# Kernel optimization log

Measured on AMD Instinct MI355X. Metric: run time of the kernel, lower is better.

The kernel has to match this reference:

```python
import jax, jax.numpy as jnp
import numpy as np

N, E = 40000, 640000          # nodes, edges (avg degree 16)
IN_N, IN_E = 8 + 768, 2       # in_dim_node + in_dim_text, in_dim_edge
H, OUT, NC, L = 128, 128, 5, 2
EPS_BN, EPS_DEN = 1e-5, 1e-6


def setup_inputs() -> dict:
    key = jax.random.key(0)
    ks = jax.random.split(key, 16)
    w = lambda k, shape: jax.random.normal(k, shape, jnp.float32) * 0.05
    return {
        "node_feat": jax.random.normal(ks[0], (N, IN_N), jnp.float32),
        "edge_feat": jax.random.normal(ks[1], (E, IN_E), jnp.float32),
        "src": jax.random.randint(ks[2], (E,), 0, N),
        "dst": jax.random.randint(ks[3], (E,), 0, N),
        "enc_nw": w(ks[4], (IN_N, H)), "enc_nb": jnp.zeros((H,), jnp.float32),
        "enc_ew": w(ks[5], (IN_E, H)), "enc_eb": jnp.zeros((H,), jnp.float32),
        # per layer: 5 linears (order A, B, C, D, E)
        "lin_w": w(ks[6], (L, 5, H, H)), "lin_b": jnp.zeros((L, 5, H), jnp.float32),
        "bnh_g": jnp.ones((L, H), jnp.float32), "bnh_b": jnp.zeros((L, H), jnp.float32),
        "bne_g": jnp.ones((L, H), jnp.float32), "bne_b": jnp.zeros((L, H), jnp.float32),
        "mlp_w1": w(ks[7], (H, OUT)), "mlp_b1": jnp.zeros((OUT,), jnp.float32),
        "mlp_w2": w(ks[8], (OUT, NC)), "mlp_b2": jnp.zeros((NC,), jnp.float32),
    }


def _bn(x, g, b):
    # training-mode BatchNorm1d: batch stats, biased variance, eps=1e-5
    m = jnp.mean(x, axis=0)
    v = jnp.var(x, axis=0)
    return (x - m) * jax.lax.rsqrt(v + EPS_BN) * g + b


def reference(node_feat, edge_feat, src, dst, enc_nw, enc_nb, enc_ew, enc_eb,
              lin_w, lin_b, bnh_g, bnh_b, bne_g, bne_b,
              mlp_w1, mlp_b1, mlp_w2, mlp_b2):
    n = node_feat.shape[0]
    h = node_feat @ enc_nw + enc_nb          # [N, H]
    e = edge_feat @ enc_ew + enc_eb          # [E, H]
    for l in range(L):
        Ah = h @ lin_w[l, 0] + lin_b[l, 0]
        Bh = h @ lin_w[l, 1] + lin_b[l, 1]
        Ce = e @ lin_w[l, 2] + lin_b[l, 2]
        Dh = h @ lin_w[l, 3] + lin_b[l, 3]
        Eh = h @ lin_w[l, 4] + lin_b[l, 4]
        e_new = Ce + Dh[src] + Eh[dst]       # [E, H] edge gate logits
        sigma = jax.nn.sigmoid(e_new)
        num = jax.ops.segment_sum(sigma * Bh[src], dst, num_segments=n)
        den = jax.ops.segment_sum(sigma, dst, num_segments=n)
        h_new = Ah + num / (den + EPS_DEN)
        h = jax.nn.relu(_bn(h_new, bnh_g[l], bnh_b[l]))
        e = jax.nn.relu(_bn(e_new, bne_g[l], bne_b[l]))
    # MLP readout per node (dropout p=0 -> identity)
    logits = jax.nn.relu(h @ mlp_w1 + mlp_b1) @ mlp_w2 + mlp_b2
    return logits
```

## Files before the change

### kernel.cpp

```cpp
#include <hip/hip_runtime.h>
#include <math.h>

#define NN 40000
#define NE 640000
#define KIN 776
#define HH 128
#define NCLS 5

typedef __attribute__((ext_vector_type(8))) short bf16x8;
typedef __attribute__((ext_vector_type(4))) short bf16x4;
typedef __attribute__((ext_vector_type(4))) float f32x4;

__device__ __forceinline__ float bf2f(short u) {
    return __uint_as_float(((unsigned)(unsigned short)u) << 16);
}
__device__ __forceinline__ short f2bf(float f) {
    unsigned u = __float_as_uint(f);
    u += 0x7fffu + ((u >> 16) & 1u);
    return (short)(u >> 16);
}

template<int NSTEP, bool TAIL8>
__global__ __launch_bounds__(256)
void mfma_gemm(const float* __restrict__ Af, const short* __restrict__ Wp,
               const float* __restrict__ bias, short* __restrict__ Cb, int K)
{
    const int lane = threadIdx.x & 63;
    const int wave = threadIdx.x >> 6;
    const int q = lane >> 4;
    const int c16 = lane & 15;
    const int row = blockIdx.x * 64 + wave * 16 + c16;

    f32x4 acc[8];
#pragma unroll
    for (int n = 0; n < 8; ++n) acc[n] = (f32x4){0.f, 0.f, 0.f, 0.f};

    for (int kt = 0; kt < NSTEP; ++kt) {
        bf16x8 afrag;
        const int kbase = kt * 32 + q * 8;
        if (!TAIL8 || kt < NSTEP - 1 || q == 0) {
            const float* p = Af + (size_t)row * K + kbase;
            const float4 x = *(const float4*)p;
            const float4 y = *(const float4*)(p + 4);
            afrag[0] = f2bf(x.x); afrag[1] = f2bf(x.y);
            afrag[2] = f2bf(x.z); afrag[3] = f2bf(x.w);
            afrag[4] = f2bf(y.x); afrag[5] = f2bf(y.y);
            afrag[6] = f2bf(y.z); afrag[7] = f2bf(y.w);
        } else {
#pragma unroll
            for (int j = 0; j < 8; ++j) afrag[j] = 0;
        }
        const int kb = kt * 4 + q;
#pragma unroll
        for (int n = 0; n < 8; ++n) {
            const bf16x8 wfrag =
                *(const bf16x8*)(Wp + (size_t)kb * 1024 + (n * 16 + c16) * 8);
            acc[n] = __builtin_amdgcn_mfma_f32_16x16x32_bf16(wfrag, afrag, acc[n], 0, 0, 0);
        }
    }
#pragma unroll
    for (int n = 0; n < 8; ++n) {
        const int col = n * 16 + q * 4;
        const float4 b4 = *(const float4*)(bias + col);
        bf16x4 o;
        o[0] = f2bf(acc[n][0] + b4.x); o[1] = f2bf(acc[n][1] + b4.y);
        o[2] = f2bf(acc[n][2] + b4.z); o[3] = f2bf(acc[n][3] + b4.w);
        *(bf16x4*)(Cb + (size_t)row * HH + col) = o;
    }
}

template<bool ABN>
__global__ __launch_bounds__(256, 2)
void fused4_k(const short* __restrict__ hb, const float* __restrict__ hf,
              const float* __restrict__ bnp,
              const short* __restrict__ w0, const short* __restrict__ w1,
              const short* __restrict__ w2, const short* __restrict__ w3,
              const float* __restrict__ b0, const float* __restrict__ b1,
              const float* __restrict__ b2, const float* __restrict__ b3,
              float* __restrict__ Ah, short* __restrict__ Bh,
              short* __restrict__ Dh, short* __restrict__ Eh)
{
    const int lane = threadIdx.x & 63;
    const int wave = threadIdx.x >> 6;
    const int q = lane >> 4;
    const int c16 = lane & 15;
    const int row = blockIdx.x * 64 + wave * 16 + c16;

    f32x4 acc[4][8];
#pragma unroll
    for (int t = 0; t < 4; ++t)
#pragma unroll
        for (int n = 0; n < 8; ++n) acc[t][n] = (f32x4){0.f, 0.f, 0.f, 0.f};

    const short* const ws[4] = {w0, w1, w2, w3};
#pragma unroll
    for (int kt = 0; kt < 4; ++kt) {
        const int kbase = kt * 32 + q * 8;
        bf16x8 afrag;
        if (!ABN) {
            afrag = *(const bf16x8*)(hb + (size_t)row * HH + kbase);
        } else {
            const float* p = hf + (size_t)row * HH + kbase;
            const float4 x = *(const float4*)p;
            const float4 y = *(const float4*)(p + 4);
            const float4 s0 = *(const float4*)(bnp + kbase);
            const float4 s1 = *(const float4*)(bnp + kbase + 4);
            const float4 t0 = *(const float4*)(bnp + HH + kbase);
            const float4 t1 = *(const float4*)(bnp + HH + kbase + 4);
            const float xv[8] = {x.x, x.y, x.z, x.w, y.x, y.y, y.z, y.w};
            const float scv[8] = {s0.x, s0.y, s0.z, s0.w, s1.x, s1.y, s1.z, s1.w};
            const float shv[8] = {t0.x, t0.y, t0.z, t0.w, t1.x, t1.y, t1.z, t1.w};
#pragma unroll
            for (int j = 0; j < 8; ++j)
                afrag[j] = f2bf(fmaxf(fmaf(xv[j], scv[j], shv[j]), 0.f));
        }
        const int kb = kt * 4 + q;
#pragma unroll
        for (int t = 0; t < 4; ++t)
#pragma unroll
            for (int n = 0; n < 8; ++n) {
                const bf16x8 wfrag =
                    *(const bf16x8*)(ws[t] + (size_t)kb * 1024 + (n * 16 + c16) * 8);
                acc[t][n] = __builtin_amdgcn_mfma_f32_16x16x32_bf16(wfrag, afrag, acc[t][n], 0, 0, 0);
            }
    }

    const float* const bs[4] = {b0, b1, b2, b3};
#pragma unroll
    for (int t = 0; t < 4; ++t) {
#pragma unroll
        for (int n = 0; n < 8; ++n) {
            const int col = n * 16 + q * 4;
            const float4 b4 = *(const float4*)(bs[t] + col);
            const float v[4] = {acc[t][n][0] + b4.x, acc[t][n][1] + b4.y,
                                acc[t][n][2] + b4.z, acc[t][n][3] + b4.w};
            if (t == 0) {
                *(float4*)(Ah + (size_t)row * HH + col) = make_float4(v[0], v[1], v[2], v[3]);
            } else {
                bf16x4 o;
#pragma unroll
                for (int j = 0; j < 4; ++j) o[j] = f2bf(v[j]);
                short* dstp = (t == 1) ? Bh : ((t == 2) ? Dh : Eh);
                *(bf16x4*)(dstp + (size_t)row * HH + col) = o;
            }
        }
    }
}

__global__ __launch_bounds__(256)
void edge1seg_k(const float* __restrict__ ef, const int* __restrict__ eidx,
                const int* __restrict__ src_s, const int* __restrict__ rowptr,
                const float* __restrict__ G,
                const short* __restrict__ Dh, const short* __restrict__ Eh,
                const short* __restrict__ Bh, const float* __restrict__ Ah,
                float* __restrict__ hnew, float* __restrict__ pbuf)
{
    const int wv = threadIdx.x >> 6;
    const int lane = threadIdx.x & 63;
    const int slot = lane >> 4;
    const int cg = lane & 15;
    const int col = cg * 8;
    const int n0 = (blockIdx.x * 4 + wv) * 8;

    const float4 g00 = *(const float4*)(G + col);
    const float4 g01 = *(const float4*)(G + col + 4);
    const float4 g10 = *(const float4*)(G + HH + col);
    const float4 g11 = *(const float4*)(G + HH + col + 4);
    const float4 gb0 = *(const float4*)(G + 2 * HH + col);
    const float4 gb1 = *(const float4*)(G + 2 * HH + col + 4);
    const float G0v[8] = {g00.x, g00.y, g00.z, g00.w, g01.x, g01.y, g01.z, g01.w};
    const float G1v[8] = {g10.x, g10.y, g10.z, g10.w, g11.x, g11.y, g11.z, g11.w};
    const float GBv[8] = {gb0.x, gb0.y, gb0.z, gb0.w, gb1.x, gb1.y, gb1.z, gb1.w};

    float esa[8] = {}, esq[8] = {};

    for (int nn = 0; nn < 8; ++nn) {
        const int n = n0 + nn;
        const int k0 = rowptr[n], k1 = rowptr[n + 1];
        const bf16x8 ehn = *(const bf16x8*)(Eh + (size_t)n * HH + col);
        float ehv[8];
#pragma unroll
        for (int j = 0; j < 8; ++j) ehv[j] = bf2f(ehn[j]);
        float num[8] = {}, den[8] = {};
        for (int k = k0 + slot; k < k1; k += 4) {
            const int e = eidx[k];
            const int s = src_s[k];
            const float f0 = ef[(size_t)e * 2];
            const float f1 = ef[(size_t)e * 2 + 1];
            const bf16x8 dh = *(const bf16x8*)(Dh + (size_t)s * HH + col);
            const bf16x8 bh = *(const bf16x8*)(Bh + (size_t)s * HH + col);
#pragma unroll
            for (int j = 0; j < 8; ++j) {
                const float v = fmaf(f0, G0v[j], fmaf(f1, G1v[j], GBv[j]))
                                + bf2f(dh[j]) + ehv[j];
                esa[j] += v; esq[j] += v * v;
                const float sg = 1.f / (1.f + __expf(-v));
                den[j] += sg;
                num[j] = fmaf(sg, bf2f(bh[j]), num[j]);
            }
        }
#pragma unroll
        for (int j = 0; j < 8; ++j) {
            num[j] += __shfl_xor(num[j], 16, 64);
            den[j] += __shfl_xor(den[j], 16, 64);
            num[j] += __shfl_xor(num[j], 32, 64);
            den[j] += __shfl_xor(den[j], 32, 64);
        }
        if (slot == 0) {
            const size_t idx = (size_t)n * HH + col;
            const float4 a0 = *(const float4*)(Ah + idx);
            const float4 a1 = *(const float4*)(Ah + idx + 4);
            const float av[8] = {a0.x, a0.y, a0.z, a0.w, a1.x, a1.y, a1.z, a1.w};
            float x[8];
#pragma unroll
            for (int j = 0; j < 8; ++j) x[j] = av[j] + num[j] / (den[j] + 1e-6f);
            *(float4*)(hnew + idx) = make_float4(x[0], x[1], x[2], x[3]);
            *(float4*)(hnew + idx + 4) = make_float4(x[4], x[5], x[6], x[7]);
        }
    }

    __shared__ float sred[16][136];
    const int er = threadIdx.x >> 4;
    const int slotp = (blockIdx.x & 63) * 256;
#pragma unroll
    for (int j = 0; j < 8; ++j) sred[er][col + j] = esa[j];
    __syncthreads();
    for (int s2 = 8; s2 > 0; s2 >>= 1) {
        if (er < s2)
#pragma unroll
            for (int j = 0; j < 8; ++j) sred[er][col + j] += sred[er + s2][col + j];
        __syncthreads();
    }
    if (er == 0)
#pragma unroll
        for (int j = 0; j < 8; ++j) atomicAdd(pbuf + slotp + col + j, sred[0][col + j]);
    __syncthreads();
#pragma unroll
    for (int j = 0; j < 8; ++j) sred[er][col + j] = esq[j];
    __syncthreads();
    for (int s2 = 8; s2 > 0; s2 >>= 1) {
        if (er < s2)
#pragma unroll
            for (int j = 0; j < 8; ++j) sred[er][col + j] += sred[er + s2][col + j];
        __syncthreads();
    }
    if (er == 0)
#pragma unroll
        for (int j = 0; j < 8; ++j) atomicAdd(pbuf + slotp + 128 + col + j, sred[0][col + j]);
}

__global__ void gm_k(const float* __restrict__ G, const float* __restrict__ bnpe,
                     float* __restrict__ Gm)
{
    const int c = threadIdx.x;
    const float sc = bnpe[c], sh = bnpe[128 + c];
    Gm[c] = G[c] * sc;
    Gm[128 + c] = G[HH + c] * sc;
    Gm[256 + c] = fmaf(G[2 * HH + c], sc, sh);
    Gm[384 + c] = sc;
}

__global__ __launch_bounds__(256)
void edge2_k(const int* __restrict__ eidx, const float* __restrict__ ef,
             const float* __restrict__ Gm,
             const short* __restrict__ Dh0, const short* __restrict__ Eh0,
             const short* __restrict__ Dh1, const short* __restrict__ Eh1,
             const int* __restrict__ src_s, const int* __restrict__ dst_s,
             const short* __restrict__ Wp, const float* __restrict__ bias,
             short* __restrict__ enew)
{
    const int lane = threadIdx.x & 63;
    const int wave = threadIdx.x >> 6;
    const int q = lane >> 4;
    const int c16 = lane & 15;
    const int row0 = blockIdx.x * 128 + wave * 16 + c16;
    const int row1 = row0 + 64;

    const int s0 = src_s[row0], d0 = dst_s[row0];
    const int s1 = src_s[row1], d1 = dst_s[row1];
    const int e0 = eidx[row0], e1 = eidx[row1];
    const float2 ef0 = *(const float2*)(ef + (size_t)e0 * 2);
    const float2 ef1 = *(const float2*)(ef + (size_t)e1 * 2);

    f32x4 acc[2][8];
#pragma unroll
    for (int n = 0; n < 8; ++n) {
        const int col = n * 16 + q * 4;
        const float4 b4 = *(const float4*)(bias + col);
        const bf16x4 dh0 = *(const bf16x4*)(Dh1 + (size_t)s0 * HH + col);
        const bf16x4 eh0 = *(const bf16x4*)(Eh1 + (size_t)d0 * HH + col);
        const bf16x4 dh1 = *(const bf16x4*)(Dh1 + (size_t)s1 * HH + col);
        const bf16x4 eh1 = *(const bf16x4*)(Eh1 + (size_t)d1 * HH + col);
        const float bb[4] = {b4.x, b4.y, b4.z, b4.w};
#pragma unroll
        for (int j = 0; j < 4; ++j) {
            acc[0][n][j] = bb[j] + bf2f(dh0[j]) + bf2f(eh0[j]);
            acc[1][n][j] = bb[j] + bf2f(dh1[j]) + bf2f(eh1[j]);
        }
    }

#pragma unroll
    for (int kt = 0; kt < 4; ++kt) {
        const int kbase = kt * 32 + q * 8;
        const float4 p0 = *(const float4*)(Gm + kbase);
        const float4 p1 = *(const float4*)(Gm + kbase + 4);
        const float4 p2 = *(const float4*)(Gm + 128 + kbase);
        const float4 p3 = *(const float4*)(Gm + 128 + kbase + 4);
        const float4 p4 = *(const float4*)(Gm + 256 + kbase);
        const float4 p5 = *(const float4*)(Gm + 256 + kbase + 4);
        const float4 p6 = *(const float4*)(Gm + 384 + kbase);
        const float4 p7 = *(const float4*)(Gm + 384 + kbase + 4);
        const float g0s[8] = {p0.x, p0.y, p0.z, p0.w, p1.x, p1.y, p1.z, p1.w};
        const float g1s[8] = {p2.x, p2.y, p2.z, p2.w, p3.x, p3.y, p3.z, p3.w};
        const float gbs[8] = {p4.x, p4.y, p4.z, p4.w, p5.x, p5.y, p5.z, p5.w};
        const float scv[8] = {p6.x, p6.y, p6.z, p6.w, p7.x, p7.y, p7.z, p7.w};
        const bf16x8 dA0 = *(const bf16x8*)(Dh0 + (size_t)s0 * HH + kbase);
        const bf16x8 eA0 = *(const bf16x8*)(Eh0 + (size_t)d0 * HH + kbase);
        const bf16x8 dA1 = *(const bf16x8*)(Dh0 + (size_t)s1 * HH + kbase);
        const bf16x8 eA1 = *(const bf16x8*)(Eh0 + (size_t)d1 * HH + kbase);
        bf16x8 a0, a1;
#pragma unroll
        for (int j = 0; j < 8; ++j) {
            float t0 = fmaf(scv[j], bf2f(dA0[j]) + bf2f(eA0[j]), gbs[j]);
            t0 = fmaf(ef0.x, g0s[j], fmaf(ef0.y, g1s[j], t0));
            a0[j] = f2bf(fmaxf(t0, 0.f));
            float t1 = fmaf(scv[j], bf2f(dA1[j]) + bf2f(eA1[j]), gbs[j]);
            t1 = fmaf(ef1.x, g0s[j], fmaf(ef1.y, g1s[j], t1));
            a1[j] = f2bf(fmaxf(t1, 0.f));
        }
        const int kb = kt * 4 + q;
#pragma unroll
        for (int n = 0; n < 8; ++n) {
            const bf16x8 wfrag =
                *(const bf16x8*)(Wp + (size_t)kb * 1024 + (n * 16 + c16) * 8);
            acc[0][n] = __builtin_amdgcn_mfma_f32_16x16x32_bf16(wfrag, a0, acc[0][n], 0, 0, 0);
            acc[1][n] = __builtin_amdgcn_mfma_f32_16x16x32_bf16(wfrag, a1, acc[1][n], 0, 0, 0);
        }
    }

#pragma unroll
    for (int n = 0; n < 8; ++n) {
        const int col = n * 16 + q * 4;
        bf16x4 o0, o1;
#pragma unroll
        for (int j = 0; j < 4; ++j) {
            o0[j] = f2bf(acc[0][n][j]);
            o1[j] = f2bf(acc[1][n][j]);
        }
        *(bf16x4*)(enew + (size_t)row0 * HH + col) = o0;
        *(bf16x4*)(enew + (size_t)row1 * HH + col) = o1;
    }
}

__global__ __launch_bounds__(256)
void seg_reduce_v(const short* __restrict__ enew, const int* __restrict__ rowptr,
                  const int* __restrict__ src_s, const short* __restrict__ Bh,
                  const float* __restrict__ Ah, float* __restrict__ hnew,
                  float* __restrict__ pbuf)
{
    const int wv = threadIdx.x >> 6;
    const int lane = threadIdx.x & 63;
    const int slot = lane >> 4;
    const int cg = lane & 15;
    const int col = cg * 8;
    const int n0 = (blockIdx.x * 4 + wv) * 8;
    float sa[8] = {}, qa[8] = {};
    for (int nn = 0; nn < 8; ++nn) {
        const int n = n0 + nn;
        const int k0 = rowptr[n], k1 = rowptr[n + 1];
        float num[8] = {}, den[8] = {};
        for (int k = k0 + slot; k < k1; k += 4) {
            const bf16x8 ev = *(const bf16x8*)(enew + (size_t)k * HH + col);
            const int s = src_s[k];
            const bf16x8 bv = *(const bf16x8*)(Bh + (size_t)s * HH + col);
#pragma unroll
            for (int j = 0; j < 8; ++j) {
                const float sg = 1.f / (1.f + __expf(-bf2f(ev[j])));
                den[j] += sg;
                num[j] = fmaf(sg, bf2f(bv[j]), num[j]);
            }
        }
#pragma unroll
        for (int j = 0; j < 8; ++j) {
            num[j] += __shfl_xor(num[j], 16, 64);
            den[j] += __shfl_xor(den[j], 16, 64);
            num[j] += __shfl_xor(num[j], 32, 64);
            den[j] += __shfl_xor(den[j], 32, 64);
        }
        if (slot == 0) {
            const size_t idx = (size_t)n * HH + col;
            const float4 a0 = *(const float4*)(Ah + idx);
            const float4 a1 = *(const float4*)(Ah + idx + 4);
            const float av[8] = {a0.x, a0.y, a0.z, a0.w, a1.x, a1.y, a1.z, a1.w};
            float x[8];
#pragma unroll
            for (int j = 0; j < 8; ++j) {
                x[j] = av[j] + num[j] / (den[j] + 1e-6f);
                sa[j] += x[j]; qa[j] += x[j] * x[j];
            }
            *(float4*)(hnew + idx) = make_float4(x[0], x[1], x[2], x[3]);
            *(float4*)(hnew + idx + 4) = make_float4(x[4], x[5], x[6], x[7]);
        }
    }
    if (slot == 0) {
        const int sl = (blockIdx.x & 63) * 256;
#pragma unroll
        for (int j = 0; j < 8; ++j) {
            atomicAdd(pbuf + sl + col + j, sa[j]);
            atomicAdd(pbuf + sl + 128 + col + j, qa[j]);
        }
    }
}

__global__ __launch_bounds__(256)
void readout_k(const float* __restrict__ hnew, const float* __restrict__ bnp,
               const short* __restrict__ Wp, const float* __restrict__ b1,
               const float* __restrict__ w2, const float* __restrict__ b2,
               float* __restrict__ out)
{
    const int lane = threadIdx.x & 63;
    const int wave = threadIdx.x >> 6;
    const int q = lane >> 4;
    const int c16 = lane & 15;
    const int row = blockIdx.x * 64 + wave * 16 + c16;

    f32x4 acc[8];
#pragma unroll
    for (int n = 0; n < 8; ++n) acc[n] = (f32x4){0.f, 0.f, 0.f, 0.f};

#pragma unroll
    for (int kt = 0; kt < 4; ++kt) {
        const int kbase = kt * 32 + q * 8;
        const float* p = hnew + (size_t)row * HH + kbase;
        const float4 x = *(const float4*)p;
        const float4 y = *(const float4*)(p + 4);
        const float4 s0 = *(const float4*)(bnp + kbase);
        const float4 s1 = *(const float4*)(bnp + kbase + 4);
        const float4 t0 = *(const float4*)(bnp + HH + kbase);
        const float4 t1 = *(const float4*)(bnp + HH + kbase + 4);
        const float xv[8] = {x.x, x.y, x.z, x.w, y.x, y.y, y.z, y.w};
        const float scv[8] = {s0.x, s0.y, s0.z, s0.w, s1.x, s1.y, s1.z, s1.w};
        const float shv[8] = {t0.x, t0.y, t0.z, t0.w, t1.x, t1.y, t1.z, t1.w};
        bf16x8 afrag;
#pragma unroll
        for (int j = 0; j < 8; ++j)
            afrag[j] = f2bf(fmaxf(fmaf(xv[j], scv[j], shv[j]), 0.f));
        const int kb = kt * 4 + q;
#pragma unroll
        for (int n = 0; n < 8; ++n) {
            const bf16x8 wfrag =
                *(const bf16x8*)(Wp + (size_t)kb * 1024 + (n * 16 + c16) * 8);
            acc[n] = __builtin_amdgcn_mfma_f32_16x16x32_bf16(wfrag, afrag, acc[n], 0, 0, 0);
        }
    }

    float part[NCLS] = {};
#pragma unroll
    for (int n = 0; n < 8; ++n) {
        const int col = n * 16 + q * 4;
        const float4 b4 = *(const float4*)(b1 + col);
        const float bb[4] = {b4.x, b4.y, b4.z, b4.w};
#pragma unroll
        for (int j = 0; j < 4; ++j) {
            const float zv = fmaxf(acc[n][j] + bb[j], 0.f);
#pragma unroll
            for (int t = 0; t < NCLS; ++t)
                part[t] = fmaf(zv, w2[(col + j) * NCLS + t], part[t]);
        }
    }
#pragma unroll
    for (int t = 0; t < NCLS; ++t) {
        part[t] += __shfl_xor(part[t], 16, 64);
        part[t] += __shfl_xor(part[t], 32, 64);
    }
    if (q == 0) {
#pragma unroll
        for (int t = 0; t < NCLS; ++t)
            out[(size_t)row * NCLS + t] = part[t] + b2[t];
    }
}

__global__ __launch_bounds__(256)
void prepack_k(const float* __restrict__ enc_nw, const float* __restrict__ lin_w,
               const float* __restrict__ mlp_w1, short* __restrict__ wp)
{
    const int t = blockIdx.x * 256 + threadIdx.x;
    if (t >= 260 * 128) return;
    const int kbg = t >> 7, col = t & 127;
    const int kb0[11]  = {0, 100, 116, 132, 148, 164, 180, 196, 212, 228, 244};
    const int psel[11] = {0, 1, 1, 1, 1, 1, 1, 1, 1, 1, 2};
    const int soff[11] = {0, 0 * 16384, 1 * 16384, 3 * 16384, 4 * 16384,
                          5 * 16384, 6 * 16384, 7 * 16384, 8 * 16384, 9 * 16384, 0};
    const int Ksrc[11] = {KIN, 128, 128, 128, 128, 128, 128, 128, 128, 128, 128};
    int e = 10;
    while (e > 0 && kbg < kb0[e]) --e;
    const float* base = (psel[e] == 0) ? enc_nw : ((psel[e] == 1) ? lin_w : mlp_w1);
    const int kbl = kbg - kb0[e];
    bf16x8 o;
#pragma unroll
    for (int j = 0; j < 8; ++j) {
        const int k = kbl * 8 + j;
        const float v = (k < Ksrc[e]) ? base[(size_t)soff[e] + (size_t)k * HH + col] : 0.f;
        o[j] = f2bf(v);
    }
    *(bf16x8*)(wp + (size_t)kbg * 1024 + col * 8) = o;
}

__global__ void gpre_k(const float* __restrict__ enc_ew, const float* __restrict__ enc_eb,
                       const float* __restrict__ Wc, const float* __restrict__ bc,
                       float* __restrict__ G)
{
    const int c = threadIdx.x;
    float a0 = 0.f, a1 = 0.f, ab = 0.f;
    for (int k = 0; k < HH; ++k) {
        const float w = Wc[k * HH + c];
        a0 = fmaf(enc_ew[k], w, a0);
        a1 = fmaf(enc_ew[HH + k], w, a1);
        ab = fmaf(enc_eb[k], w, ab);
    }
    G[c] = a0; G[HH + c] = a1; G[2 * HH + c] = ab + bc[c];
}

__global__ __launch_bounds__(256)
void hist_k(const int* __restrict__ dst, int* __restrict__ cnt)
{
    const int e = blockIdx.x * 256 + threadIdx.x;
    if (e < NE) atomicAdd(cnt + dst[e], 1);
}

__global__ __launch_bounds__(1024)
void scan_k(const int* __restrict__ cnt, int* __restrict__ rowptr, int* __restrict__ wr)
{
    __shared__ int s[1024];
    const int t = threadIdx.x;
    const int base = t * 40;
    int sum = 0;
    for (int i = 0; i < 40; ++i) {
        const int idx = base + i;
        if (idx < NN) sum += cnt[idx];
    }
    s[t] = sum;
    __syncthreads();
    for (int off = 1; off < 1024; off <<= 1) {
        const int v = (t >= off) ? s[t - off] : 0;
        __syncthreads();
        s[t] += v;
        __syncthreads();
    }
    int run = (t == 0) ? 0 : s[t - 1];
    for (int i = 0; i < 40; ++i) {
        const int idx = base + i;
        if (idx < NN) {
            rowptr[idx] = run;
            wr[idx] = run;
            run += cnt[idx];
        }
    }
    if (t == 1023) rowptr[NN] = s[1023];
}

__global__ __launch_bounds__(256)
void scatter_k(const int* __restrict__ dst, const int* __restrict__ src,
               int* __restrict__ wr, int* __restrict__ eidx,
               int* __restrict__ src_s, int* __restrict__ dst_s)
{
    const int e = blockIdx.x * 256 + threadIdx.x;
    if (e < NE) {
        const int d = dst[e];
        const int p = atomicAdd(wr + d, 1);
        eidx[p] = e;
        src_s[p] = src[e];
        dst_s[p] = d;
    }
}

__global__ __launch_bounds__(256)
void hstats_k(const float* __restrict__ hnew, float* __restrict__ pbuf)
{
    const int tid = threadIdx.x;
    const int c = tid & 127, sub = tid >> 7;
    const int r0 = blockIdx.x * 256;
    float sa = 0.f, qa = 0.f;
    for (int i = sub; i < 256; i += 2) {
        const int r = r0 + i;
        if (r >= NN) break;
        const float x = hnew[(size_t)r * HH + c];
        sa += x; qa += x * x;
    }
    __shared__ float red[256];
    red[tid] = sa; __syncthreads();
    if (tid < 128) atomicAdd(pbuf + (blockIdx.x & 63) * 256 + c, red[tid] + red[tid + 128]);
    __syncthreads();
    red[tid] = qa; __syncthreads();
    if (tid < 128) atomicAdd(pbuf + (blockIdx.x & 63) * 256 + 128 + c, red[tid] + red[tid + 128]);
}

__global__ void make_bnp2(const float* __restrict__ pbuf, const float* __restrict__ g,
                          const float* __restrict__ b, float cntInv,
                          float* __restrict__ out)
{
    const int c = threadIdx.x;
    float s = 0.f, q = 0.f;
    for (int i = 0; i < 64; ++i) {
        s += pbuf[i * 256 + c];
        q += pbuf[i * 256 + 128 + c];
    }
    const float m = s * cntInv;
    const float var = q * cntInv - m * m;
    const float rs = rsqrtf(var + 1e-5f);
    const float sc = g[c] * rs;
    out[c] = sc;
    out[128 + c] = b[c] - m * sc;
}

extern "C" void kernel_launch(void* const* d_in, const int* in_sizes, int n_in,
                              void* d_out, int out_size, void* d_ws, size_t ws_size,
                              hipStream_t stream)
{
    const float* node_feat = (const float*)d_in[0];
    const float* edge_feat = (const float*)d_in[1];
    const int*   src       = (const int*)d_in[2];
    const int*   dst       = (const int*)d_in[3];
    const float* enc_nw    = (const float*)d_in[4];
    const float* enc_nb    = (const float*)d_in[5];
    const float* enc_ew    = (const float*)d_in[6];
    const float* enc_eb    = (const float*)d_in[7];
    const float* lin_w     = (const float*)d_in[8];
    const float* lin_b     = (const float*)d_in[9];
    const float* bnh_g     = (const float*)d_in[10];
    const float* bnh_b     = (const float*)d_in[11];
    const float* bne_g     = (const float*)d_in[12];
    const float* bne_b     = (const float*)d_in[13];
    const float* mlp_w1    = (const float*)d_in[14];
    const float* mlp_b1    = (const float*)d_in[15];
    const float* mlp_w2    = (const float*)d_in[16];
    const float* mlp_b2    = (const float*)d_in[17];
    float* out = (float*)d_out;

    char* base = (char*)d_ws;
    size_t off = 0;
    auto alloc = [&](size_t bytes) -> void* {
        void* p = base + off;
        off = (off + bytes + 255) & ~(size_t)255;
        return p;
    };
    const size_t NH = (size_t)NN * HH;
    float* hnew  = (float*)alloc(NH * 4);
    float* Ah    = (float*)alloc(NH * 4);
    short* h0    = (short*)alloc(NH * 2);
    short* Bh0   = (short*)alloc(NH * 2);
    short* Dh0   = (short*)alloc(NH * 2);
    short* Eh0   = (short*)alloc(NH * 2);
    short* Dh1   = (short*)alloc(NH * 2);
    short* Eh1   = (short*)alloc(NH * 2);
    short* enew  = (short*)alloc((size_t)NE * HH * 2);
    short* wpack = (short*)alloc((size_t)260 * 1024 * 2);
    float* G     = (float*)alloc(384 * 4);
    float* Gm    = (float*)alloc(512 * 4);
    float* bnpe  = (float*)alloc(256 * 4);
    float* bnph  = (float*)alloc(256 * 4);
    float* pbe   = (float*)alloc(16384 * 4);
    float* pbh0  = (float*)alloc(16384 * 4);
    float* pbh1  = (float*)alloc(16384 * 4);
    int* cnt     = (int*)alloc(NN * 4);
    int* rowptr  = (int*)alloc((NN + 1) * 4);
    int* wr      = (int*)alloc(NN * 4);
    int* eidx    = (int*)alloc((size_t)NE * 4);
    int* src_s   = (int*)alloc((size_t)NE * 4);
    int* dst_s   = (int*)alloc((size_t)NE * 4);

    const dim3 blk(256);

    hipMemsetAsync(cnt, 0, NN * 4, stream);
    hipMemsetAsync(pbe, 0, 3 * 16384 * 4, stream);
    hist_k<<<2500, blk, 0, stream>>>(dst, cnt);
    scan_k<<<1, 1024, 0, stream>>>(cnt, rowptr, wr);
    scatter_k<<<2500, blk, 0, stream>>>(dst, src, wr, eidx, src_s, dst_s);
    prepack_k<<<130, blk, 0, stream>>>(enc_nw, lin_w, mlp_w1, wpack);
    gpre_k<<<1, 128, 0, stream>>>(enc_ew, enc_eb, lin_w + 2 * 16384, lin_b + 2 * HH, G);

    mfma_gemm<25, true><<<625, blk, 0, stream>>>(node_feat, wpack, enc_nb, h0, KIN);

    {
        const float* Bv = lin_b;
        fused4_k<false><<<625, blk, 0, stream>>>(
            h0, nullptr, nullptr,
            wpack + (size_t)100 * 1024, wpack + (size_t)116 * 1024,
            wpack + (size_t)132 * 1024, wpack + (size_t)148 * 1024,
            Bv + 0 * HH, Bv + 1 * HH, Bv + 3 * HH, Bv + 4 * HH,
            Ah, Bh0, Dh0, Eh0);
        edge1seg_k<<<1250, blk, 0, stream>>>(edge_feat, eidx, src_s, rowptr, G,
                                             Dh0, Eh0, Bh0, Ah, hnew, pbe);
        make_bnp2<<<1, 128, 0, stream>>>(pbe, bne_g, bne_b, 1.f / NE, bnpe);
        gm_k<<<1, 128, 0, stream>>>(G, bnpe, Gm);
        hstats_k<<<157, blk, 0, stream>>>(hnew, pbh0);
        make_bnp2<<<1, 128, 0, stream>>>(pbh0, bnh_g, bnh_b, 1.f / NN, bnph);
    }

    {
        const float* Bv = lin_b + 5 * HH;
        short* Bh1 = h0;
        fused4_k<true><<<625, blk, 0, stream>>>(
            nullptr, hnew, bnph,
            wpack + (size_t)164 * 1024, wpack + (size_t)180 * 1024,
            wpack + (size_t)212 * 1024, wpack + (size_t)228 * 1024,
            Bv + 0 * HH, Bv + 1 * HH, Bv + 3 * HH, Bv + 4 * HH,
            Ah, Bh1, Dh1, Eh1);
        edge2_k<<<5000, blk, 0, stream>>>(eidx, edge_feat, Gm, Dh0, Eh0, Dh1, Eh1,
                                          src_s, dst_s, wpack + (size_t)196 * 1024,
                                          Bv + 2 * HH, enew);
        seg_reduce_v<<<1250, blk, 0, stream>>>(enew, rowptr, src_s, Bh1, Ah, hnew, pbh1);
        make_bnp2<<<1, 128, 0, stream>>>(pbh1, bnh_g + HH, bnh_b + HH, 1.f / NN, bnph);
    }

    readout_k<<<625, blk, 0, stream>>>(hnew, bnph, wpack + (size_t)244 * 1024,
                                       mlp_b1, mlp_w2, mlp_b2, out);
}
```

Before: 854.7 us.

## Fuse h BN stats into edge kernel, pre-sort edge features, unroll segment loops

The edge features are gathered into destination-sorted order during the scatter pass, so the edge kernels read them contiguously instead of going through an edge-index indirection. The layer-1 node batch-norm statistics are now accumulated inside the edge segment kernel, which removes the separate hstats pass over hnew. The Gm computation is folded into make_bnp2, removing one tiny launch. The segment loops are unrolled by two to keep more gathers in flight, and each wave handles 4 nodes instead of 8, doubling the grid. The costs are a scatter of an extra 8 bytes per edge and a longer reduction tail in the edge kernel.

```diff
diff --git a/kernel.cpp b/kernel.cpp
--- a/kernel.cpp
+++ b/kernel.cpp
@@ -148,19 +148,19 @@
 }
 
 __global__ __launch_bounds__(256)
-void edge1seg_k(const float* __restrict__ ef, const int* __restrict__ eidx,
-                const int* __restrict__ src_s, const int* __restrict__ rowptr,
-                const float* __restrict__ G,
+void edge1seg_k(const float2* __restrict__ ef_s, const int* __restrict__ src_s,
+                const int* __restrict__ rowptr, const float* __restrict__ G,
                 const short* __restrict__ Dh, const short* __restrict__ Eh,
                 const short* __restrict__ Bh, const float* __restrict__ Ah,
-                float* __restrict__ hnew, float* __restrict__ pbuf)
+                float* __restrict__ hnew, float* __restrict__ pbe,
+                float* __restrict__ pbh)
 {
     const int wv = threadIdx.x >> 6;
     const int lane = threadIdx.x & 63;
     const int slot = lane >> 4;
     const int cg = lane & 15;
     const int col = cg * 8;
-    const int n0 = (blockIdx.x * 4 + wv) * 8;
+    const int n0 = (blockIdx.x * 4 + wv) * 4;
 
     const float4 g00 = *(const float4*)(G + col);
     const float4 g01 = *(const float4*)(G + col + 4);
@@ -173,8 +173,9 @@
     const float GBv[8] = {gb0.x, gb0.y, gb0.z, gb0.w, gb1.x, gb1.y, gb1.z, gb1.w};
 
     float esa[8] = {}, esq[8] = {};
-
-    for (int nn = 0; nn < 8; ++nn) {
+    float hsa[8] = {}, hsq[8] = {};
+
+    for (int nn = 0; nn < 4; ++nn) {
         const int n = n0 + nn;
         const int k0 = rowptr[n], k1 = rowptr[n + 1];
         const bf16x8 ehn = *(const bf16x8*)(Eh + (size_t)n * HH + col);
@@ -182,21 +183,45 @@
 #pragma unroll
         for (int j = 0; j < 8; ++j) ehv[j] = bf2f(ehn[j]);
         float num[8] = {}, den[8] = {};
-        for (int k = k0 + slot; k < k1; k += 4) {
-            const int e = eidx[k];
-            const int s = src_s[k];
-            const float f0 = ef[(size_t)e * 2];
-            const float f1 = ef[(size_t)e * 2 + 1];
-            const bf16x8 dh = *(const bf16x8*)(Dh + (size_t)s * HH + col);
-            const bf16x8 bh = *(const bf16x8*)(Bh + (size_t)s * HH + col);
+        int k = k0 + slot;
+        for (; k + 4 < k1; k += 8) {
+            const float2 fA = ef_s[k];
+            const int sA = src_s[k];
+            const float2 fB = ef_s[k + 4];
+            const int sB = src_s[k + 4];
+            const bf16x8 dhA = *(const bf16x8*)(Dh + (size_t)sA * HH + col);
+            const bf16x8 bhA = *(const bf16x8*)(Bh + (size_t)sA * HH + col);
+            const bf16x8 dhB = *(const bf16x8*)(Dh + (size_t)sB * HH + col);
+            const bf16x8 bhB = *(const bf16x8*)(Bh + (size_t)sB * HH + col);
 #pragma unroll
             for (int j = 0; j < 8; ++j) {
-                const float v = fmaf(f0, G0v[j], fmaf(f1, G1v[j], GBv[j]))
-                                + bf2f(dh[j]) + ehv[j];
+                float v = fmaf(fA.x, G0v[j], fmaf(fA.y, G1v[j], GBv[j]))
+                          + bf2f(dhA[j]) + ehv[j];
+                esa[j] += v; esq[j] += v * v;
+                float sg = 1.f / (1.f + __expf(-v));
+                den[j] += sg;
+                num[j] = fmaf(sg, bf2f(bhA[j]), num[j]);
+                v = fmaf(fB.x, G0v[j], fmaf(fB.y, G1v[j], GBv[j]))
+                    + bf2f(dhB[j]) + ehv[j];
+                esa[j] += v; esq[j] += v * v;
+                sg = 1.f / (1.f + __expf(-v));
+                den[j] += sg;
+                num[j] = fmaf(sg, bf2f(bhB[j]), num[j]);
+            }
+        }
+        if (k < k1) {
+            const float2 fA = ef_s[k];
+            const int sA = src_s[k];
+            const bf16x8 dhA = *(const bf16x8*)(Dh + (size_t)sA * HH + col);
+            const bf16x8 bhA = *(const bf16x8*)(Bh + (size_t)sA * HH + col);
+#pragma unroll
+            for (int j = 0; j < 8; ++j) {
+                const float v = fmaf(fA.x, G0v[j], fmaf(fA.y, G1v[j], GBv[j]))
+                                + bf2f(dhA[j]) + ehv[j];
                 esa[j] += v; esq[j] += v * v;
                 const float sg = 1.f / (1.f + __expf(-v));
                 den[j] += sg;
-                num[j] = fmaf(sg, bf2f(bh[j]), num[j]);
+                num[j] = fmaf(sg, bf2f(bhA[j]), num[j]);
             }
         }
 #pragma unroll
@@ -213,7 +238,10 @@
             const float av[8] = {a0.x, a0.y, a0.z, a0.w, a1.x, a1.y, a1.z, a1.w};
             float x[8];
 #pragma unroll
-            for (int j = 0; j < 8; ++j) x[j] = av[j] + num[j] / (den[j] + 1e-6f);
+            for (int j = 0; j < 8; ++j) {
+                x[j] = av[j] + num[j] / (den[j] + 1e-6f);
+                hsa[j] += x[j]; hsq[j] += x[j] * x[j];
+            }
             *(float4*)(hnew + idx) = make_float4(x[0], x[1], x[2], x[3]);
             *(float4*)(hnew + idx + 4) = make_float4(x[4], x[5], x[6], x[7]);
         }
@@ -223,46 +251,31 @@
     const int er = threadIdx.x >> 4;
     const int slotp = (blockIdx.x & 63) * 256;
 #pragma unroll
-    for (int j = 0; j < 8; ++j) sred[er][col + j] = esa[j];
-    __syncthreads();
-    for (int s2 = 8; s2 > 0; s2 >>= 1) {
-        if (er < s2)
-#pragma unroll
-            for (int j = 0; j < 8; ++j) sred[er][col + j] += sred[er + s2][col + j];
+    for (int pass = 0; pass < 4; ++pass) {
+        const float* srcv = (pass == 0) ? esa : (pass == 1) ? esq
+                           : (pass == 2) ? hsa : hsq;
         __syncthreads();
-    }
-    if (er == 0)
-#pragma unroll
-        for (int j = 0; j < 8; ++j) atomicAdd(pbuf + slotp + col + j, sred[0][col + j]);
-    __syncthreads();
-#pragma unroll
-    for (int j = 0; j < 8; ++j) sred[er][col + j] = esq[j];
-    __syncthreads();
-    for (int s2 = 8; s2 > 0; s2 >>= 1) {
-        if (er < s2)
-#pragma unroll
-            for (int j = 0; j < 8; ++j) sred[er][col + j] += sred[er + s2][col + j];
+#pragma unroll
+        for (int j = 0; j < 8; ++j) sred[er][col + j] = srcv[j];
         __syncthreads();
-    }
-    if (er == 0)
-#pragma unroll
-        for (int j = 0; j < 8; ++j) atomicAdd(pbuf + slotp + 128 + col + j, sred[0][col + j]);
-}
-
-__global__ void gm_k(const float* __restrict__ G, const float* __restrict__ bnpe,
-                     float* __restrict__ Gm)
-{
-    const int c = threadIdx.x;
-    const float sc = bnpe[c], sh = bnpe[128 + c];
-    Gm[c] = G[c] * sc;
-    Gm[128 + c] = G[HH + c] * sc;
-    Gm[256 + c] = fmaf(G[2 * HH + c], sc, sh);
-    Gm[384 + c] = sc;
+        for (int s2 = 8; s2 > 0; s2 >>= 1) {
+            if (er < s2)
+#pragma unroll
+                for (int j = 0; j < 8; ++j) sred[er][col + j] += sred[er + s2][col + j];
+            __syncthreads();
+        }
+        if (er == 0) {
+            float* dstp = (pass < 2) ? pbe : pbh;
+            const int o = (pass & 1) ? 128 : 0;
+#pragma unroll
+            for (int j = 0; j < 8; ++j)
+                atomicAdd(dstp + slotp + o + col + j, sred[0][col + j]);
+        }
+    }
 }
 
 __global__ __launch_bounds__(256)
-void edge2_k(const int* __restrict__ eidx, const float* __restrict__ ef,
-             const float* __restrict__ Gm,
+void edge2_k(const float2* __restrict__ ef_s, const float* __restrict__ Gm,
              const short* __restrict__ Dh0, const short* __restrict__ Eh0,
              const short* __restrict__ Dh1, const short* __restrict__ Eh1,
              const int* __restrict__ src_s, const int* __restrict__ dst_s,
@@ -278,9 +291,8 @@
 
     const int s0 = src_s[row0], d0 = dst_s[row0];
     const int s1 = src_s[row1], d1 = dst_s[row1];
-    const int e0 = eidx[row0], e1 = eidx[row1];
-    const float2 ef0 = *(const float2*)(ef + (size_t)e0 * 2);
-    const float2 ef1 = *(const float2*)(ef + (size_t)e1 * 2);
+    const float2 ef0 = ef_s[row0];
+    const float2 ef1 = ef_s[row1];
 
     f32x4 acc[2][8];
 #pragma unroll
@@ -363,13 +375,31 @@
     const int slot = lane >> 4;
     const int cg = lane & 15;
     const int col = cg * 8;
-    const int n0 = (blockIdx.x * 4 + wv) * 8;
+    const int n0 = (blockIdx.x * 4 + wv) * 4;
     float sa[8] = {}, qa[8] = {};
-    for (int nn = 0; nn < 8; ++nn) {
+    for (int nn = 0; nn < 4; ++nn) {
         const int n = n0 + nn;
         const int k0 = rowptr[n], k1 = rowptr[n + 1];
         float num[8] = {}, den[8] = {};
-        for (int k = k0 + slot; k < k1; k += 4) {
+        int k = k0 + slot;
+        for (; k + 4 < k1; k += 8) {
+            const bf16x8 evA = *(const bf16x8*)(enew + (size_t)k * HH + col);
+            const int sA = src_s[k];
+            const bf16x8 evB = *(const bf16x8*)(enew + (size_t)(k + 4) * HH + col);
+            const int sB = src_s[k + 4];
+            const bf16x8 bvA = *(const bf16x8*)(Bh + (size_t)sA * HH + col);
+            const bf16x8 bvB = *(const bf16x8*)(Bh + (size_t)sB * HH + col);
+#pragma unroll
+            for (int j = 0; j < 8; ++j) {
+                float sg = 1.f / (1.f + __expf(-bf2f(evA[j])));
+                den[j] += sg;
+                num[j] = fmaf(sg, bf2f(bvA[j]), num[j]);
+                sg = 1.f / (1.f + __expf(-bf2f(evB[j])));
+                den[j] += sg;
+                num[j] = fmaf(sg, bf2f(bvB[j]), num[j]);
+            }
+        }
+        if (k < k1) {
             const bf16x8 ev = *(const bf16x8*)(enew + (size_t)k * HH + col);
             const int s = src_s[k];
             const bf16x8 bv = *(const bf16x8*)(Bh + (size_t)s * HH + col);
@@ -561,43 +591,25 @@
 
 __global__ __launch_bounds__(256)
 void scatter_k(const int* __restrict__ dst, const int* __restrict__ src,
-               int* __restrict__ wr, int* __restrict__ eidx,
-               int* __restrict__ src_s, int* __restrict__ dst_s)
+               const float* __restrict__ ef, int* __restrict__ wr,
+               int* __restrict__ src_s, int* __restrict__ dst_s,
+               float2* __restrict__ ef_s)
 {
     const int e = blockIdx.x * 256 + threadIdx.x;
     if (e < NE) {
         const int d = dst[e];
         const int p = atomicAdd(wr + d, 1);
-        eidx[p] = e;
         src_s[p] = src[e];
         dst_s[p] = d;
-    }
-}
-
-__global__ __launch_bounds__(256)
-void hstats_k(const float* __restrict__ hnew, float* __restrict__ pbuf)
-{
-    const int tid = threadIdx.x;
-    const int c = tid & 127, sub = tid >> 7;
-    const int r0 = blockIdx.x * 256;
-    float sa = 0.f, qa = 0.f;
-    for (int i = sub; i < 256; i += 2) {
-        const int r = r0 + i;
-        if (r >= NN) break;
-        const float x = hnew[(size_t)r * HH + c];
-        sa += x; qa += x * x;
-    }
-    __shared__ float red[256];
-    red[tid] = sa; __syncthreads();
-    if (tid < 128) atomicAdd(pbuf + (blockIdx.x & 63) * 256 + c, red[tid] + red[tid + 128]);
-    __syncthreads();
-    red[tid] = qa; __syncthreads();
-    if (tid < 128) atomicAdd(pbuf + (blockIdx.x & 63) * 256 + 128 + c, red[tid] + red[tid + 128]);
-}
-
+        ef_s[p] = ((const float2*)ef)[e];
+    }
+}
+
+template<bool DOGM>
 __global__ void make_bnp2(const float* __restrict__ pbuf, const float* __restrict__ g,
                           const float* __restrict__ b, float cntInv,
-                          float* __restrict__ out)
+                          float* __restrict__ out, const float* __restrict__ G,
+                          float* __restrict__ Gm)
 {
     const int c = threadIdx.x;
     float s = 0.f, q = 0.f;
@@ -609,8 +621,15 @@
     const float var = q * cntInv - m * m;
     const float rs = rsqrtf(var + 1e-5f);
     const float sc = g[c] * rs;
+    const float sh = b[c] - m * sc;
     out[c] = sc;
-    out[128 + c] = b[c] - m * sc;
+    out[128 + c] = sh;
+    if (DOGM) {
+        Gm[c] = G[c] * sc;
+        Gm[128 + c] = G[HH + c] * sc;
+        Gm[256 + c] = fmaf(G[2 * HH + c], sc, sh);
+        Gm[384 + c] = sc;
+    }
 }
 
 extern "C" void kernel_launch(void* const* d_in, const int* in_sizes, int n_in,
@@ -665,9 +684,9 @@
     int* cnt     = (int*)alloc(NN * 4);
     int* rowptr  = (int*)alloc((NN + 1) * 4);
     int* wr      = (int*)alloc(NN * 4);
-    int* eidx    = (int*)alloc((size_t)NE * 4);
     int* src_s   = (int*)alloc((size_t)NE * 4);
     int* dst_s   = (int*)alloc((size_t)NE * 4);
+    float2* ef_s = (float2*)alloc((size_t)NE * 8);
 
     const dim3 blk(256);
 
@@ -675,7 +694,7 @@
     hipMemsetAsync(pbe, 0, 3 * 16384 * 4, stream);
     hist_k<<<2500, blk, 0, stream>>>(dst, cnt);
     scan_k<<<1, 1024, 0, stream>>>(cnt, rowptr, wr);
-    scatter_k<<<2500, blk, 0, stream>>>(dst, src, wr, eidx, src_s, dst_s);
+    scatter_k<<<2500, blk, 0, stream>>>(dst, src, edge_feat, wr, src_s, dst_s, ef_s);
     prepack_k<<<130, blk, 0, stream>>>(enc_nw, lin_w, mlp_w1, wpack);
     gpre_k<<<1, 128, 0, stream>>>(enc_ew, enc_eb, lin_w + 2 * 16384, lin_b + 2 * HH, G);
 
@@ -689,12 +708,11 @@
             wpack + (size_t)132 * 1024, wpack + (size_t)148 * 1024,
             Bv + 0 * HH, Bv + 1 * HH, Bv + 3 * HH, Bv + 4 * HH,
             Ah, Bh0, Dh0, Eh0);
-        edge1seg_k<<<1250, blk, 0, stream>>>(edge_feat, eidx, src_s, rowptr, G,
-                                             Dh0, Eh0, Bh0, Ah, hnew, pbe);
-        make_bnp2<<<1, 128, 0, stream>>>(pbe, bne_g, bne_b, 1.f / NE, bnpe);
-        gm_k<<<1, 128, 0, stream>>>(G, bnpe, Gm);
-        hstats_k<<<157, blk, 0, stream>>>(hnew, pbh0);
-        make_bnp2<<<1, 128, 0, stream>>>(pbh0, bnh_g, bnh_b, 1.f / NN, bnph);
+        edge1seg_k<<<2500, blk, 0, stream>>>(ef_s, src_s, rowptr, G,
+                                             Dh0, Eh0, Bh0, Ah, hnew, pbe, pbh0);
+        make_bnp2<true><<<1, 128, 0, stream>>>(pbe, bne_g, bne_b, 1.f / NE, bnpe, G, Gm);
+        make_bnp2<false><<<1, 128, 0, stream>>>(pbh0, bnh_g, bnh_b, 1.f / NN, bnph,
+                                                nullptr, nullptr);
     }
 
     {
@@ -706,11 +724,12 @@
             wpack + (size_t)212 * 1024, wpack + (size_t)228 * 1024,
             Bv + 0 * HH, Bv + 1 * HH, Bv + 3 * HH, Bv + 4 * HH,
             Ah, Bh1, Dh1, Eh1);
-        edge2_k<<<5000, blk, 0, stream>>>(eidx, edge_feat, Gm, Dh0, Eh0, Dh1, Eh1,
+        edge2_k<<<5000, blk, 0, stream>>>(ef_s, Gm, Dh0, Eh0, Dh1, Eh1,
                                           src_s, dst_s, wpack + (size_t)196 * 1024,
                                           Bv + 2 * HH, enew);
-        seg_reduce_v<<<1250, blk, 0, stream>>>(enew, rowptr, src_s, Bh1, Ah, hnew, pbh1);
-        make_bnp2<<<1, 128, 0, stream>>>(pbh1, bnh_g + HH, bnh_b + HH, 1.f / NN, bnph);
+        seg_reduce_v<<<2500, blk, 0, stream>>>(enew, rowptr, src_s, Bh1, Ah, hnew, pbh1);
+        make_bnp2<false><<<1, 128, 0, stream>>>(pbh1, bnh_g + HH, bnh_b + HH, 1.f / NN,
+                                                bnph, nullptr, nullptr);
     }
 
     readout_k<<<625, blk, 0, stream>>>(hnew, bnph, wpack + (size_t)244 * 1024,
```

Measured after the change: 778.9 us. 8.9% less time.
